# Performance work log

Hardware: AMD Instinct MI355X
Metric: run time of the kernel (lower is better)

## Reference

```python
import jax, jax.numpy as jnp
import numpy as np

B, S, D = 16, 512, 768      # batch, max_n_words, context_dim (input_size)
E, R = 128, 2048            # entities per doc, candidate relations per doc
H = 768                     # config.hidden_size
H2 = H // 2                 # 384
OUT = 2                     # binary relation classes


def _linear_params(k, fan_in, fan_out):
    k1, k2 = jax.random.split(k)
    bound = 1.0 / np.sqrt(fan_in)
    W = jax.random.uniform(k1, (fan_in, fan_out), minval=-bound, maxval=bound, dtype=jnp.float32)
    b = jax.random.uniform(k2, (fan_out,), minval=-bound, maxval=bound, dtype=jnp.float32)
    return W, b


def setup_inputs() -> dict:
    key = jax.random.key(0)
    ks = jax.random.split(key, 16)
    hW1, hb1 = _linear_params(ks[0], 2 * D, H)
    hW2, hb2 = _linear_params(ks[1], H, H2)
    tW1, tb1 = _linear_params(ks[2], 2 * D, H)
    tW2, tb2 = _linear_params(ks[3], H, H2)
    bnd = 1.0 / np.sqrt(H2)
    bil_w = jax.random.uniform(ks[4], (OUT, H2, H2), minval=-bnd, maxval=bnd, dtype=jnp.float32)
    lW, lb = _linear_params(ks[5], 2 * H2, OUT)
    emb = jax.random.normal(ks[6], (3, D), dtype=jnp.float32)  # entity_emb
    hidden_states = jax.random.normal(ks[7], (B, S, D), dtype=jnp.float32)
    ent_start = jax.random.randint(ks[8], (B, E), 0, S)
    ent_label = jax.random.randint(ks[9], (B, E), 0, 3)
    rel_head = jax.random.randint(ks[10], (B, R), 0, E)
    rel_tail = jax.random.randint(ks[11], (B, R), 0, E)
    rel_label = jax.random.randint(ks[12], (B, R), 0, 2)
    return dict(hidden_states=hidden_states, emb=emb,
                hW1=hW1, hb1=hb1, hW2=hW2, hb2=hb2,
                tW1=tW1, tb1=tb1, tW2=tW2, tb2=tb2,
                bil_w=bil_w, lW=lW, lb=lb,
                ent_start=ent_start, ent_label=ent_label,
                rel_head=rel_head, rel_tail=rel_tail, rel_label=rel_label)


def reference(hidden_states, emb, hW1, hb1, hW2, hb2, tW1, tb1, tW2, tb2,
              bil_w, lW, lb, ent_start, ent_label, rel_head, rel_tail, rel_label):
    def tower(rel_idx, W1, b1, W2, b2):
        start = jnp.take_along_axis(ent_start, rel_idx, axis=1)              # [B,R]
        lab = jnp.take_along_axis(ent_label, rel_idx, axis=1)                # [B,R]
        hid = jnp.take_along_axis(hidden_states, start[..., None], axis=1)   # [B,R,D]
        rep = jnp.concatenate([hid, emb[lab]], axis=-1)                      # [B,R,2D]
        h = jax.nn.relu(rep @ W1 + b1)                                       # [B,R,H]
        return jax.nn.relu(h @ W2 + b2)                                      # [B,R,H2]

    heads = tower(rel_head, hW1, hb1, hW2, hb2)
    tails = tower(rel_tail, tW1, tb1, tW2, tb2)
    # Biaffine: bilinear (no bias) + linear over concat
    logits = (jnp.einsum('bri,oij,brj->bro', heads, bil_w, tails)
              + jnp.concatenate([heads, tails], axis=-1) @ lW + lb)          # [B,R,2]
    logp = jax.nn.log_softmax(logits, axis=-1)
    loss = -jnp.mean(jnp.take_along_axis(logp, rel_label[..., None], axis=-1))
    return loss, logits
```

## Files before the change

kernel.cpp:

```cpp
#include <hip/hip_runtime.h>
#include <hip/hip_bf16.h>
#include <cstdint>

typedef unsigned short ushort_t;
typedef __bf16 bf16x8 __attribute__((ext_vector_type(8)));
typedef float f32x4 __attribute__((ext_vector_type(4)));

#define B_   16
#define S_   512
#define D_   768
#define E_   128

__device__ inline ushort_t f2b(float f) {
    uint32_t u = __builtin_bit_cast(uint32_t, f);
    uint32_t r = (u + 0x7fffu + ((u >> 16) & 1u)) >> 16;
    return (ushort_t)r;
}
__device__ inline float b2f(ushort_t u) {
    uint32_t v = ((uint32_t)u) << 16;
    return __builtin_bit_cast(float, v);
}
__device__ inline float bl(uint32_t u) {
    uint32_t v = u << 16;
    return __builtin_bit_cast(float, v);
}
__device__ inline float bh(uint32_t u) {
    uint32_t v = u & 0xffff0000u;
    return __builtin_bit_cast(float, v);
}

__global__ __launch_bounds__(256) void prep_all(
    const float* __restrict__ hidden, const float* __restrict__ emb,
    const float* __restrict__ hW1, const float* __restrict__ tW1,
    const float* __restrict__ hW2, const float* __restrict__ tW2,
    const float* __restrict__ bil, const float* __restrict__ lW,
    const int* __restrict__ ent_start, const int* __restrict__ ent_label,
    ushort_t* __restrict__ repE, ushort_t* __restrict__ hW1T, ushort_t* __restrict__ tW1T,
    ushort_t* __restrict__ hW2T, ushort_t* __restrict__ tW2T,
    ushort_t* __restrict__ BmatT, ushort_t* __restrict__ lWtT, float* __restrict__ out)
{
    __shared__ float tp[32][33];
    const int u = blockIdx.x, t = threadIdx.x;
    if (u == 0 && t == 0) out[0] = 0.0f;

    if (u < 3072) {
        int idx = u * 256 + t;
        int row = idx / 384, q = idx - row * 384;
        int c = q * 4;
        int b = row >> 7;
        int st = ent_start[row], lab = ent_label[row];
        const float* srcp = (c < 768)
            ? hidden + ((size_t)(b * S_ + st) * D_ + c)
            : emb + ((size_t)lab * D_ + (c - 768));
        float4 v = *reinterpret_cast<const float4*>(srcp);
        uint32_t lo = (uint32_t)f2b(v.x) | ((uint32_t)f2b(v.y) << 16);
        uint32_t hi = (uint32_t)f2b(v.z) | ((uint32_t)f2b(v.w) << 16);
        uint2 pk; pk.x = lo; pk.y = hi;
        *reinterpret_cast<uint2*>(repE + (size_t)idx * 4) = pk;
        return;
    }
    if (u < 6240) {
        int u2 = u - 3072;
        const float* src; ushort_t* dst; int Rr, Cc, base;
        if (u2 < 1152)      { src = hW1;          dst = hW1T;           Rr = 1536; Cc = 768; base = 0; }
        else if (u2 < 2304) { src = tW1;          dst = tW1T;           Rr = 1536; Cc = 768; base = 1152; }
        else if (u2 < 2592) { src = hW2;          dst = hW2T;           Rr = 768;  Cc = 384; base = 2304; }
        else if (u2 < 2880) { src = tW2;          dst = tW2T;           Rr = 768;  Cc = 384; base = 2592; }
        else if (u2 < 3024) { src = bil;          dst = BmatT;          Rr = 384;  Cc = 384; base = 2880; }
        else                { src = bil + 147456; dst = BmatT + 147456; Rr = 384;  Cc = 384; base = 3024; }
        int local = u2 - base, nC = Cc >> 5;
        int tR = (local / nC) * 32, tC = (local - (local / nC) * nC) * 32;
        int tx = t & 31, ty = t >> 5;
#pragma unroll
        for (int r = 0; r < 4; ++r)
            tp[ty + r * 8][tx] = src[(size_t)(tR + ty + r * 8) * Cc + tC + tx];
        __syncthreads();
#pragma unroll
        for (int r = 0; r < 4; ++r)
            dst[(size_t)(tC + ty + r * 8) * Rr + tR + tx] = f2b(tp[tx][ty + r * 8]);
        return;
    }
    int i2 = (u - 6240) * 256 + t;
    if (i2 < 768) {
        int o = i2 / 384, kk = i2 - o * 384;
        BmatT[(768 + o) * 384 + kk] = f2b(lW[kk * 2 + o]);
    } else if (i2 < 1536) {
        int j = i2 - 768;
        int o = j / 384, ii = j - o * 384;
        lWtT[o * 384 + ii] = f2b(lW[(384 + ii) * 2 + o]);
    }
}

__global__ __launch_bounds__(256) void gemm_lds(
    const ushort_t* __restrict__ A0, const ushort_t* __restrict__ A1,
    const ushort_t* __restrict__ Bt0, const ushort_t* __restrict__ Bt1,
    const float* __restrict__ bias0, const float* __restrict__ bias1,
    ushort_t* __restrict__ out0, ushort_t* __restrict__ out1,
    int M, int N, int K, int doRelu)
{
    __shared__ ushort_t As[64 * 32];
    __shared__ ushort_t Bs[64 * 32];
    const ushort_t* A   = blockIdx.z ? A1 : A0;
    const ushort_t* Bt  = blockIdx.z ? Bt1 : Bt0;
    const float*   bias = blockIdx.z ? bias1 : bias0;
    ushort_t*      out  = blockIdx.z ? out1 : out0;

    int t = threadIdx.x;
    int lane = t & 63, wave = t >> 6;
    int tileM = blockIdx.x * 64, tileN = blockIdx.y * 64;
    int wm = (wave >> 1) * 32, wn = (wave & 1) * 32;
    int l15 = lane & 15, quad = lane >> 4;
    int srow = t >> 2, sc8 = (t & 3) << 3;

    const ushort_t* gA = A  + (size_t)tileM * K;
    const ushort_t* gB = Bt + (size_t)tileN * K;

    f32x4 acc[2][2];
#pragma unroll
    for (int a = 0; a < 2; ++a)
#pragma unroll
        for (int b = 0; b < 2; ++b) {
            acc[a][b][0] = 0.f; acc[a][b][1] = 0.f;
            acc[a][b][2] = 0.f; acc[a][b][3] = 0.f;
        }

    for (int k0 = 0; k0 < K; k0 += 32) {
        __builtin_amdgcn_global_load_lds(
            (const __attribute__((address_space(1))) void*)(gA + (size_t)srow * K + k0 + sc8),
            (__attribute__((address_space(3))) void*)(As + t * 8), 16, 0, 0);
        __builtin_amdgcn_global_load_lds(
            (const __attribute__((address_space(1))) void*)(gB + (size_t)srow * K + k0 + sc8),
            (__attribute__((address_space(3))) void*)(Bs + t * 8), 16, 0, 0);
        __syncthreads();
        bf16x8 af[2], bfr[2];
#pragma unroll
        for (int mi = 0; mi < 2; ++mi)
            af[mi] = *reinterpret_cast<const bf16x8*>(As + (wm + mi * 16 + l15) * 32 + quad * 8);
#pragma unroll
        for (int ni = 0; ni < 2; ++ni)
            bfr[ni] = *reinterpret_cast<const bf16x8*>(Bs + (wn + ni * 16 + l15) * 32 + quad * 8);
#pragma unroll
        for (int mi = 0; mi < 2; ++mi)
#pragma unroll
            for (int ni = 0; ni < 2; ++ni)
                acc[mi][ni] = __builtin_amdgcn_mfma_f32_16x16x32_bf16(af[mi], bfr[ni], acc[mi][ni], 0, 0, 0);
        __syncthreads();
    }

#pragma unroll
    for (int mi = 0; mi < 2; ++mi) {
        int gr = tileM + wm + mi * 16 + quad * 4;
#pragma unroll
        for (int ni = 0; ni < 2; ++ni) {
            int gc = tileN + wn + ni * 16 + l15;
            if (gc < N) {
                float bb = bias ? bias[gc] : 0.0f;
#pragma unroll
                for (int r = 0; r < 4; ++r) {
                    float v = acc[mi][ni][r] + bb;
                    if (doRelu) v = fmaxf(v, 0.0f);
                    out[(size_t)(gr + r) * N + gc] = f2b(v);
                }
            }
        }
    }
}

__global__ __launch_bounds__(256) void gemm3_tail(
    const ushort_t* __restrict__ headsE, const ushort_t* __restrict__ BmatT,
    const ushort_t* __restrict__ tailsE, const ushort_t* __restrict__ lWtT,
    ushort_t* __restrict__ Uext, float* __restrict__ tailLin)
{
    const int t = threadIdx.x;
    if (blockIdx.y == 13) {
        int r = blockIdx.x * 64 + (t >> 2), q = t & 3;
        const uint32_t* tv = reinterpret_cast<const uint32_t*>(tailsE + (size_t)r * 384);
        const uint32_t* lw = reinterpret_cast<const uint32_t*>(lWtT);
        float p0 = 0.f, p1 = 0.f;
#pragma unroll 8
        for (int i = q * 48; i < q * 48 + 48; ++i) {
            uint32_t tu = tv[i];
            float tl = bl(tu), th = bh(tu);
            uint32_t l0 = lw[i], l1 = lw[192 + i];
            p0 += tl * bl(l0) + th * bh(l0);
            p1 += tl * bl(l1) + th * bh(l1);
        }
        p0 += __shfl_xor(p0, 1); p0 += __shfl_xor(p0, 2);
        p1 += __shfl_xor(p1, 1); p1 += __shfl_xor(p1, 2);
        if (q == 0) tailLin[2 * r]     = p0;
        if (q == 1) tailLin[2 * r + 1] = p1;
        return;
    }

    __shared__ ushort_t As[64 * 32];
    __shared__ ushort_t Bs[64 * 32];
    const int K = 384, N = 770;
    int lane = t & 63, wave = t >> 6;
    int tileM = blockIdx.x * 64, tileN = blockIdx.y * 64;
    int wm = (wave >> 1) * 32, wn = (wave & 1) * 32;
    int l15 = lane & 15, quad = lane >> 4;
    int srow = t >> 2, sc8 = (t & 3) << 3;

    const ushort_t* gA = headsE + (size_t)tileM * K;
    const ushort_t* gB = BmatT  + (size_t)tileN * K;

    f32x4 acc[2][2];
#pragma unroll
    for (int a = 0; a < 2; ++a)
#pragma unroll
        for (int b = 0; b < 2; ++b) {
            acc[a][b][0] = 0.f; acc[a][b][1] = 0.f;
            acc[a][b][2] = 0.f; acc[a][b][3] = 0.f;
        }

    for (int k0 = 0; k0 < K; k0 += 32) {
        __builtin_amdgcn_global_load_lds(
            (const __attribute__((address_space(1))) void*)(gA + (size_t)srow * K + k0 + sc8),
            (__attribute__((address_space(3))) void*)(As + t * 8), 16, 0, 0);
        __builtin_amdgcn_global_load_lds(
            (const __attribute__((address_space(1))) void*)(gB + (size_t)srow * K + k0 + sc8),
            (__attribute__((address_space(3))) void*)(Bs + t * 8), 16, 0, 0);
        __syncthreads();
        bf16x8 af[2], bfr[2];
#pragma unroll
        for (int mi = 0; mi < 2; ++mi)
            af[mi] = *reinterpret_cast<const bf16x8*>(As + (wm + mi * 16 + l15) * 32 + quad * 8);
#pragma unroll
        for (int ni = 0; ni < 2; ++ni)
            bfr[ni] = *reinterpret_cast<const bf16x8*>(Bs + (wn + ni * 16 + l15) * 32 + quad * 8);
#pragma unroll
        for (int mi = 0; mi < 2; ++mi)
#pragma unroll
            for (int ni = 0; ni < 2; ++ni)
                acc[mi][ni] = __builtin_amdgcn_mfma_f32_16x16x32_bf16(af[mi], bfr[ni], acc[mi][ni], 0, 0, 0);
        __syncthreads();
    }

#pragma unroll
    for (int mi = 0; mi < 2; ++mi) {
        int gr = tileM + wm + mi * 16 + quad * 4;
#pragma unroll
        for (int ni = 0; ni < 2; ++ni) {
            int gc = tileN + wn + ni * 16 + l15;
            if (gc < N) {
#pragma unroll
                for (int r = 0; r < 4; ++r)
                    Uext[(size_t)(gr + r) * N + gc] = f2b(acc[mi][ni][r]);
            }
        }
    }
}

__global__ __launch_bounds__(256) void rel16_kernel(
    const ushort_t* __restrict__ Uext, const ushort_t* __restrict__ tailsE,
    const float* __restrict__ tailLin, const float* __restrict__ lb,
    const int* __restrict__ rel_head, const int* __restrict__ rel_tail,
    const int* __restrict__ rel_label, float* __restrict__ out)
{
    __shared__ float wsum[4];
    const int t = threadIdx.x;
    int lane = t & 63, wave = t >> 6;
    int l = lane & 15, g = lane >> 4;
    float lb0 = lb[0], lb1 = lb[1];
    float lossAcc = 0.0f;

    int rel = (blockIdx.x * 4 + wave) * 4 + g;
    int b = rel >> 11;
    int h = rel_head[rel], tt = rel_tail[rel], lab = rel_label[rel];
    const uint32_t* uh = reinterpret_cast<const uint32_t*>(Uext + (size_t)(b * E_ + h) * 770);
    const uint32_t* tv = reinterpret_cast<const uint32_t*>(tailsE + (size_t)(b * E_ + tt) * 384);
    float a0 = 0.f, a1 = 0.f;
#pragma unroll
    for (int j = 0; j < 12; ++j) {
        int i = l + 16 * j;
        uint32_t tu = tv[i];
        float tl = bl(tu), th = bh(tu);
        uint32_t u0 = uh[i], u1 = uh[192 + i];
        a0 += tl * bl(u0) + th * bh(u0);
        a1 += tl * bl(u1) + th * bh(u1);
    }
#pragma unroll
    for (int d = 1; d < 16; d <<= 1) {
        a0 += __shfl_xor(a0, d);
        a1 += __shfl_xor(a1, d);
    }
    if (l == 0) {
        const ushort_t* uhs = reinterpret_cast<const ushort_t*>(uh);
        int te = b * E_ + tt;
        float l0v = a0 + tailLin[2 * te]     + b2f(uhs[768]) + lb0;
        float l1v = a1 + tailLin[2 * te + 1] + b2f(uhs[769]) + lb1;
        out[1 + 2 * rel]     = l0v;
        out[1 + 2 * rel + 1] = l1v;
        float m = fmaxf(l0v, l1v);
        lossAcc = m + logf(expf(l0v - m) + expf(l1v - m)) - (lab ? l1v : l0v);
    }
    lossAcc += __shfl_xor(lossAcc, 16);
    lossAcc += __shfl_xor(lossAcc, 32);
    if (lane == 0) wsum[wave] = lossAcc;
    __syncthreads();
    if (t == 0)
        atomicAdd(out, (wsum[0] + wsum[1] + wsum[2] + wsum[3]) * (1.0f / 32768.0f));
}

extern "C" void kernel_launch(void* const* d_in, const int* in_sizes, int n_in,
                              void* d_out, int out_size, void* d_ws, size_t ws_size,
                              hipStream_t stream)
{
    const float* hidden = (const float*)d_in[0];
    const float* emb    = (const float*)d_in[1];
    const float* hW1    = (const float*)d_in[2];
    const float* hb1    = (const float*)d_in[3];
    const float* hW2    = (const float*)d_in[4];
    const float* hb2    = (const float*)d_in[5];
    const float* tW1    = (const float*)d_in[6];
    const float* tb1    = (const float*)d_in[7];
    const float* tW2    = (const float*)d_in[8];
    const float* tb2    = (const float*)d_in[9];
    const float* bil    = (const float*)d_in[10];
    const float* lW     = (const float*)d_in[11];
    const float* lb     = (const float*)d_in[12];
    const int* ent_start = (const int*)d_in[13];
    const int* ent_label = (const int*)d_in[14];
    const int* rel_head  = (const int*)d_in[15];
    const int* rel_tail  = (const int*)d_in[16];
    const int* rel_label = (const int*)d_in[17];
    float* out = (float*)d_out;

    char* ws = (char*)d_ws;
    ushort_t* repE   = (ushort_t*)(ws + 0);
    ushort_t* hW1T   = (ushort_t*)(ws + 6291456);
    ushort_t* tW1T   = (ushort_t*)(ws + 8650752);
    ushort_t* hW2T   = (ushort_t*)(ws + 11010048);
    ushort_t* tW2T   = (ushort_t*)(ws + 11599872);
    ushort_t* BmatT  = (ushort_t*)(ws + 12189696);
    ushort_t* lWtT   = (ushort_t*)(ws + 12781056);
    ushort_t* h1     = (ushort_t*)(ws + 12782592);
    ushort_t* t1     = (ushort_t*)(ws + 15928320);
    ushort_t* headsE = (ushort_t*)(ws + 19074048);
    ushort_t* tailsE = (ushort_t*)(ws + 20646912);
    ushort_t* Uext   = (ushort_t*)(ws + 22219776);
    float*    tailLin= (float*)   (ws + 25373696);

    prep_all<<<6246, 256, 0, stream>>>(
        hidden, emb, hW1, tW1, hW2, tW2, bil, lW, ent_start, ent_label,
        repE, hW1T, tW1T, hW2T, tW2T, BmatT, lWtT, out);

    gemm_lds<<<dim3(32, 12, 2), 256, 0, stream>>>(
        repE, repE, hW1T, tW1T, hb1, tb1, h1, t1, 2048, 768, 1536, 1);

    gemm_lds<<<dim3(32, 6, 2), 256, 0, stream>>>(
        h1, t1, hW2T, tW2T, hb2, tb2, headsE, tailsE, 2048, 384, 768, 1);

    gemm3_tail<<<dim3(32, 14, 1), 256, 0, stream>>>(
        headsE, BmatT, tailsE, lWtT, Uext, tailLin);

    rel16_kernel<<<2048, 256, 0, stream>>>(
        Uext, tailsE, tailLin, lb, rel_head, rel_tail, rel_label, out);
}
```

Measured before the change: 181.6 us.

## Precompute embedding-times-W1 table to halve first GEMM K dimension

New measurement: 241.1 us. 1.33x slower.

```diff
diff --git a/kernel.cpp b/kernel.cpp
--- a/kernel.cpp
+++ b/kernel.cpp
@@ -10,6 +10,7 @@
 #define S_   512
 #define D_   768
 #define E_   128
+#define USTRIDE 784
 
 __device__ inline ushort_t f2b(float f) {
     uint32_t u = __builtin_bit_cast(uint32_t, f);
@@ -37,21 +38,20 @@
     const int* __restrict__ ent_start, const int* __restrict__ ent_label,
     ushort_t* __restrict__ repE, ushort_t* __restrict__ hW1T, ushort_t* __restrict__ tW1T,
     ushort_t* __restrict__ hW2T, ushort_t* __restrict__ tW2T,
-    ushort_t* __restrict__ BmatT, ushort_t* __restrict__ lWtT, float* __restrict__ out)
+    ushort_t* __restrict__ BmatT, ushort_t* __restrict__ lWtT,
+    float* __restrict__ embW1, float* __restrict__ out)
 {
     __shared__ float tp[32][33];
     const int u = blockIdx.x, t = threadIdx.x;
     if (u == 0 && t == 0) out[0] = 0.0f;
 
-    if (u < 3072) {
+    if (u < 1536) {
         int idx = u * 256 + t;
-        int row = idx / 384, q = idx - row * 384;
+        int row = idx / 192, q = idx - row * 192;
         int c = q * 4;
         int b = row >> 7;
-        int st = ent_start[row], lab = ent_label[row];
-        const float* srcp = (c < 768)
-            ? hidden + ((size_t)(b * S_ + st) * D_ + c)
-            : emb + ((size_t)lab * D_ + (c - 768));
+        int st = ent_start[row];
+        const float* srcp = hidden + ((size_t)(b * S_ + st) * D_ + c);
         float4 v = *reinterpret_cast<const float4*>(srcp);
         uint32_t lo = (uint32_t)f2b(v.x) | ((uint32_t)f2b(v.y) << 16);
         uint32_t hi = (uint32_t)f2b(v.z) | ((uint32_t)f2b(v.w) << 16);
@@ -59,16 +59,25 @@
         *reinterpret_cast<uint2*>(repE + (size_t)idx * 4) = pk;
         return;
     }
-    if (u < 6240) {
-        int u2 = u - 3072;
-        const float* src; ushort_t* dst; int Rr, Cc, base;
-        if (u2 < 1152)      { src = hW1;          dst = hW1T;           Rr = 1536; Cc = 768; base = 0; }
-        else if (u2 < 2304) { src = tW1;          dst = tW1T;           Rr = 1536; Cc = 768; base = 1152; }
-        else if (u2 < 2592) { src = hW2;          dst = hW2T;           Rr = 768;  Cc = 384; base = 2304; }
-        else if (u2 < 2880) { src = tW2;          dst = tW2T;           Rr = 768;  Cc = 384; base = 2592; }
-        else if (u2 < 3024) { src = bil;          dst = BmatT;          Rr = 384;  Cc = 384; base = 2880; }
-        else                { src = bil + 147456; dst = BmatT + 147456; Rr = 384;  Cc = 384; base = 3024; }
-        int local = u2 - base, nC = Cc >> 5;
+    if (u < 3552) {
+        const float* src; ushort_t* dst; int Rr, Cc, local;
+        if (u < 2688) {
+            int u2 = u - 1536;
+            int tower = u2 / 576; local = u2 - tower * 576;
+            src = tower ? tW1 : hW1; dst = tower ? tW1T : hW1T;
+            Rr = 768; Cc = 768;
+        } else if (u < 3264) {
+            int u2 = u - 2688;
+            int tower = u2 / 288; local = u2 - tower * 288;
+            src = tower ? tW2 : hW2; dst = tower ? tW2T : hW2T;
+            Rr = 768; Cc = 384;
+        } else {
+            int u2 = u - 3264;
+            int half = u2 / 144; local = u2 - half * 144;
+            src = bil + (size_t)half * 147456; dst = BmatT + (size_t)half * 147456;
+            Rr = 384; Cc = 384;
+        }
+        int nC = Cc >> 5;
         int tR = (local / nC) * 32, tC = (local - (local / nC) * nC) * 32;
         int tx = t & 31, ty = t >> 5;
 #pragma unroll
@@ -80,7 +89,23 @@
             dst[(size_t)(tC + ty + r * 8) * Rr + tR + tx] = f2b(tp[tx][ty + r * 8]);
         return;
     }
-    int i2 = (u - 6240) * 256 + t;
+    if (u < 3570) {
+        int e = u - 3552;
+        int z = e / 9, rem = e - z * 9;
+        int lab = rem / 3, sub = rem - lab * 3;
+        const float* W1 = z ? tW1 : hW1;
+        int n = sub * 256 + t;
+        float acc = 0.0f;
+#pragma unroll 4
+        for (int k = 0; k < 768; ++k) {
+            float eb = b2f(f2b(emb[lab * D_ + k]));
+            float wb = b2f(f2b(W1[(size_t)(768 + k) * 768 + n]));
+            acc = fmaf(eb, wb, acc);
+        }
+        embW1[(size_t)(z * 3 + lab) * 768 + n] = acc;
+        return;
+    }
+    int i2 = (u - 3570) * 256 + t;
     if (i2 < 768) {
         int o = i2 / 384, kk = i2 - o * 384;
         BmatT[(768 + o) * 384 + kk] = f2b(lW[kk * 2 + o]);
@@ -91,12 +116,89 @@
     }
 }
 
+__global__ __launch_bounds__(256) void gemm1(
+    const ushort_t* __restrict__ repE,
+    const ushort_t* __restrict__ hW1T, const ushort_t* __restrict__ tW1T,
+    const float* __restrict__ hb1, const float* __restrict__ tb1,
+    const float* __restrict__ embW1, const int* __restrict__ ent_label,
+    ushort_t* __restrict__ h1, ushort_t* __restrict__ t1)
+{
+    __shared__ ushort_t As[64 * 32];
+    __shared__ ushort_t Bs[64 * 32];
+    const int K = 768, N = 768;
+    const ushort_t* Bt  = blockIdx.z ? tW1T : hW1T;
+    const float*   bias = blockIdx.z ? tb1 : hb1;
+    const float*   emb1 = embW1 + (size_t)blockIdx.z * 3 * 768;
+    ushort_t*      out  = blockIdx.z ? t1 : h1;
+
+    int t = threadIdx.x;
+    int lane = t & 63, wave = t >> 6;
+    int tileM = blockIdx.x * 64, tileN = blockIdx.y * 64;
+    int wm = (wave >> 1) * 32, wn = (wave & 1) * 32;
+    int l15 = lane & 15, quad = lane >> 4;
+    int srow = t >> 2, sc8 = (t & 3) << 3;
+
+    const ushort_t* gA = repE + (size_t)tileM * K;
+    const ushort_t* gB = Bt   + (size_t)tileN * K;
+
+    f32x4 acc[2][2];
+#pragma unroll
+    for (int a = 0; a < 2; ++a)
+#pragma unroll
+        for (int b = 0; b < 2; ++b) {
+            acc[a][b][0] = 0.f; acc[a][b][1] = 0.f;
+            acc[a][b][2] = 0.f; acc[a][b][3] = 0.f;
+        }
+
+    for (int k0 = 0; k0 < K; k0 += 32) {
+        __builtin_amdgcn_global_load_lds(
+            (const __attribute__((address_space(1))) void*)(gA + (size_t)srow * K + k0 + sc8),
+            (__attribute__((address_space(3))) void*)(As + t * 8), 16, 0, 0);
+        __builtin_amdgcn_global_load_lds(
+            (const __attribute__((address_space(1))) void*)(gB + (size_t)srow * K + k0 + sc8),
+            (__attribute__((address_space(3))) void*)(Bs + t * 8), 16, 0, 0);
+        __syncthreads();
+        bf16x8 af[2], bfr[2];
+#pragma unroll
+        for (int mi = 0; mi < 2; ++mi)
+            af[mi] = *reinterpret_cast<const bf16x8*>(As + (wm + mi * 16 + l15) * 32 + quad * 8);
+#pragma unroll
+        for (int ni = 0; ni < 2; ++ni)
+            bfr[ni] = *reinterpret_cast<const bf16x8*>(Bs + (wn + ni * 16 + l15) * 32 + quad * 8);
+#pragma unroll
+        for (int mi = 0; mi < 2; ++mi)
+#pragma unroll
+            for (int ni = 0; ni < 2; ++ni)
+                acc[mi][ni] = __builtin_amdgcn_mfma_f32_16x16x32_bf16(af[mi], bfr[ni], acc[mi][ni], 0, 0, 0);
+        __syncthreads();
+    }
+
+#pragma unroll
+    for (int mi = 0; mi < 2; ++mi) {
+        int gr = tileM + wm + mi * 16 + quad * 4;
+        int lab[4];
+#pragma unroll
+        for (int r = 0; r < 4; ++r) lab[r] = ent_label[gr + r];
+#pragma unroll
+        for (int ni = 0; ni < 2; ++ni) {
+            int gc = tileN + wn + ni * 16 + l15;
+            float bb = bias[gc];
+#pragma unroll
+            for (int r = 0; r < 4; ++r) {
+                float v = acc[mi][ni][r] + bb + emb1[(size_t)lab[r] * 768 + gc];
+                v = fmaxf(v, 0.0f);
+                out[(size_t)(gr + r) * N + gc] = f2b(v);
+            }
+        }
+    }
+}
+
 __global__ __launch_bounds__(256) void gemm_lds(
     const ushort_t* __restrict__ A0, const ushort_t* __restrict__ A1,
     const ushort_t* __restrict__ Bt0, const ushort_t* __restrict__ Bt1,
     const float* __restrict__ bias0, const float* __restrict__ bias1,
     ushort_t* __restrict__ out0, ushort_t* __restrict__ out1,
-    int M, int N, int K, int doRelu)
+    int M, int N, int K)
 {
     __shared__ ushort_t As[64 * 32];
     __shared__ ushort_t Bs[64 * 32];
@@ -154,11 +256,10 @@
         for (int ni = 0; ni < 2; ++ni) {
             int gc = tileN + wn + ni * 16 + l15;
             if (gc < N) {
-                float bb = bias ? bias[gc] : 0.0f;
+                float bb = bias[gc];
 #pragma unroll
                 for (int r = 0; r < 4; ++r) {
-                    float v = acc[mi][ni][r] + bb;
-                    if (doRelu) v = fmaxf(v, 0.0f);
+                    float v = fmaxf(acc[mi][ni][r] + bb, 0.0f);
                     out[(size_t)(gr + r) * N + gc] = f2b(v);
                 }
             }
@@ -245,7 +346,7 @@
             if (gc < N) {
 #pragma unroll
                 for (int r = 0; r < 4; ++r)
-                    Uext[(size_t)(gr + r) * N + gc] = f2b(acc[mi][ni][r]);
+                    Uext[(size_t)(gr + r) * USTRIDE + gc] = f2b(acc[mi][ni][r]);
             }
         }
     }
@@ -267,17 +368,23 @@
     int rel = (blockIdx.x * 4 + wave) * 4 + g;
     int b = rel >> 11;
     int h = rel_head[rel], tt = rel_tail[rel], lab = rel_label[rel];
-    const uint32_t* uh = reinterpret_cast<const uint32_t*>(Uext + (size_t)(b * E_ + h) * 770);
-    const uint32_t* tv = reinterpret_cast<const uint32_t*>(tailsE + (size_t)(b * E_ + tt) * 384);
+    const uint4* uh4 = reinterpret_cast<const uint4*>(Uext + (size_t)(b * E_ + h) * USTRIDE);
+    const uint4* tv4 = reinterpret_cast<const uint4*>(tailsE + (size_t)(b * E_ + tt) * 384);
     float a0 = 0.f, a1 = 0.f;
 #pragma unroll
-    for (int j = 0; j < 12; ++j) {
+    for (int j = 0; j < 3; ++j) {
         int i = l + 16 * j;
-        uint32_t tu = tv[i];
-        float tl = bl(tu), th = bh(tu);
-        uint32_t u0 = uh[i], u1 = uh[192 + i];
-        a0 += tl * bl(u0) + th * bh(u0);
-        a1 += tl * bl(u1) + th * bh(u1);
+        uint4 tu = tv4[i];
+        uint4 u0 = uh4[i];
+        uint4 u1 = uh4[48 + i];
+        a0 += bl(tu.x) * bl(u0.x) + bh(tu.x) * bh(u0.x);
+        a0 += bl(tu.y) * bl(u0.y) + bh(tu.y) * bh(u0.y);
+        a0 += bl(tu.z) * bl(u0.z) + bh(tu.z) * bh(u0.z);
+        a0 += bl(tu.w) * bl(u0.w) + bh(tu.w) * bh(u0.w);
+        a1 += bl(tu.x) * bl(u1.x) + bh(tu.x) * bh(u1.x);
+        a1 += bl(tu.y) * bl(u1.y) + bh(tu.y) * bh(u1.y);
+        a1 += bl(tu.z) * bl(u1.z) + bh(tu.z) * bh(u1.z);
+        a1 += bl(tu.w) * bl(u1.w) + bh(tu.w) * bh(u1.w);
     }
 #pragma unroll
     for (int d = 1; d < 16; d <<= 1) {
@@ -285,7 +392,7 @@
         a1 += __shfl_xor(a1, d);
     }
     if (l == 0) {
-        const ushort_t* uhs = reinterpret_cast<const ushort_t*>(uh);
+        const ushort_t* uhs = Uext + (size_t)(b * E_ + h) * USTRIDE;
         int te = b * E_ + tt;
         float l0v = a0 + tailLin[2 * te]     + b2f(uhs[768]) + lb0;
         float l1v = a1 + tailLin[2 * te + 1] + b2f(uhs[769]) + lb1;
@@ -328,28 +435,29 @@
 
     char* ws = (char*)d_ws;
     ushort_t* repE   = (ushort_t*)(ws + 0);
-    ushort_t* hW1T   = (ushort_t*)(ws + 6291456);
-    ushort_t* tW1T   = (ushort_t*)(ws + 8650752);
-    ushort_t* hW2T   = (ushort_t*)(ws + 11010048);
-    ushort_t* tW2T   = (ushort_t*)(ws + 11599872);
-    ushort_t* BmatT  = (ushort_t*)(ws + 12189696);
-    ushort_t* lWtT   = (ushort_t*)(ws + 12781056);
-    ushort_t* h1     = (ushort_t*)(ws + 12782592);
-    ushort_t* t1     = (ushort_t*)(ws + 15928320);
-    ushort_t* headsE = (ushort_t*)(ws + 19074048);
-    ushort_t* tailsE = (ushort_t*)(ws + 20646912);
-    ushort_t* Uext   = (ushort_t*)(ws + 22219776);
-    float*    tailLin= (float*)   (ws + 25373696);
-
-    prep_all<<<6246, 256, 0, stream>>>(
+    ushort_t* hW1T   = (ushort_t*)(ws + 3145728);
+    ushort_t* tW1T   = (ushort_t*)(ws + 4325376);
+    ushort_t* hW2T   = (ushort_t*)(ws + 5505024);
+    ushort_t* tW2T   = (ushort_t*)(ws + 6094848);
+    ushort_t* BmatT  = (ushort_t*)(ws + 6684672);
+    ushort_t* lWtT   = (ushort_t*)(ws + 7276032);
+    float*    embW1  = (float*)   (ws + 7277568);
+    ushort_t* h1     = (ushort_t*)(ws + 7296000);
+    ushort_t* t1     = (ushort_t*)(ws + 10441728);
+    ushort_t* headsE = (ushort_t*)(ws + 13587456);
+    ushort_t* tailsE = (ushort_t*)(ws + 15160320);
+    ushort_t* Uext   = (ushort_t*)(ws + 16733184);
+    float*    tailLin= (float*)   (ws + 19944448);
+
+    prep_all<<<3576, 256, 0, stream>>>(
         hidden, emb, hW1, tW1, hW2, tW2, bil, lW, ent_start, ent_label,
-        repE, hW1T, tW1T, hW2T, tW2T, BmatT, lWtT, out);
-
-    gemm_lds<<<dim3(32, 12, 2), 256, 0, stream>>>(
-        repE, repE, hW1T, tW1T, hb1, tb1, h1, t1, 2048, 768, 1536, 1);
+        repE, hW1T, tW1T, hW2T, tW2T, BmatT, lWtT, embW1, out);
+
+    gemm1<<<dim3(32, 12, 2), 256, 0, stream>>>(
+        repE, hW1T, tW1T, hb1, tb1, embW1, ent_label, h1, t1);
 
     gemm_lds<<<dim3(32, 6, 2), 256, 0, stream>>>(
-        h1, t1, hW2T, tW2T, hb2, tb2, headsE, tailsE, 2048, 384, 768, 1);
+        h1, t1, hW2T, tW2T, hb2, tb2, headsE, tailsE, 2048, 384, 768);
 
     gemm3_tail<<<dim3(32, 14, 1), 256, 0, stream>>>(
         headsE, BmatT, tailsE, lWtT, Uext, tailLin);
```
